# Optimization experiments

Hardware: AMD Instinct MI355X
Metric: run time of the kernel (lower is better)

## Reference

```python
import jax, jax.numpy as jnp
import numpy as np

D_K = 64
EPS = 1e-6


def setup_inputs() -> dict:
    key = jax.random.key(0)
    ks = jax.random.split(key, 6)
    B, S, D2, DV = 4, 2048, 1024, 64
    q = jax.random.normal(ks[0], (B, S, D2), dtype=jnp.float32)
    k = jax.random.normal(ks[1], (B, S, D2), dtype=jnp.float32)
    v = jax.random.normal(ks[2], (B, S, D2), dtype=jnp.float32)
    mask = jax.random.randint(ks[3], (B, S, S), 0, 2) == 1
    V = jax.random.normal(ks[4], (1, DV), dtype=jnp.float32)
    fc_w = jax.random.normal(ks[5], (D2, DV), dtype=jnp.float32) * (1.0 / np.sqrt(DV))
    fc_b = jnp.zeros((D2,), dtype=jnp.float32)
    ln_g = jnp.ones((D2,), dtype=jnp.float32)
    ln_b = jnp.zeros((D2,), dtype=jnp.float32)
    return {"q": q, "k": k, "v": v, "mask": mask, "V": V,
            "fc_w": fc_w, "fc_b": fc_b, "ln_g": ln_g, "ln_b": ln_b}


def _layer_norm(x, g, b):
    mu = jnp.mean(x, axis=-1, keepdims=True)
    var = jnp.var(x, axis=-1, keepdims=True)
    return (x - mu) * jax.lax.rsqrt(var + EPS) * g + b


def reference(q, k, v, mask, V, fc_w, fc_b, ln_g, ln_b):
    residual = q
    qn = _layer_norm(q, ln_g, ln_b)
    # scaled dot-product scores (no softmax in this variant)
    attn = jnp.einsum('bsd,btd->bst', qn / jnp.sqrt(jnp.float32(D_K)), k)
    attn = jnp.where(mask, 0.0, attn)  # masked_fill with 0
    # v_ = V broadcast over (batch, seq, key); attn @ v_ == row-sum outer V
    output = jnp.sum(attn, axis=-1, keepdims=True) * V  # [B,S,d_v]
    output = output @ fc_w.T + fc_b                     # [B,S,2*d_model]
    output = output + residual
    return (output, attn)
```

## Files before the change

### kernel.cpp

```cpp
#include <hip/hip_runtime.h>
#include <hip/hip_bf16.h>
#include <cstdint>

#define S_LEN 2048
#define D2_   1024
#define DV_   64
#define NB_   4

typedef __bf16 bf16x8 __attribute__((ext_vector_type(8)));
typedef float  f32x4  __attribute__((ext_vector_type(4)));
typedef int    i32x4  __attribute__((ext_vector_type(4)));

__device__ __forceinline__ unsigned short f2bf(float f) {
  union { float f; unsigned int u; } v; v.f = f;
  unsigned int r = v.u + 0x7fffu + ((v.u >> 16) & 1u);
  return (unsigned short)(r >> 16);
}

__device__ __forceinline__ void async16(const unsigned short* g, unsigned short* l) {
  __builtin_amdgcn_global_load_lds(
      (__attribute__((address_space(1))) void*)g,
      (__attribute__((address_space(3))) void*)l,
      16, 0, 0);
}

__global__ void __launch_bounds__(256) prep_kernel(
    const float* __restrict__ q, const float* __restrict__ k,
    const float* __restrict__ gam, const float* __restrict__ bet,
    const float* __restrict__ V, const float* __restrict__ fw,
    unsigned short* __restrict__ qn, unsigned short* __restrict__ kb,
    float* __restrict__ w2, float* __restrict__ rowsum) {
  const int row = blockIdx.x;
  const int t = threadIdx.x;

  if (row < 32) rowsum[row * 256 + t] = 0.0f;

  const float4 x = ((const float4*)(q + (size_t)row * D2_))[t];
  float s  = x.x + x.y + x.z + x.w;
  float ss = x.x * x.x + x.y * x.y + x.z * x.z + x.w * x.w;
  #pragma unroll
  for (int o = 32; o > 0; o >>= 1) { s += __shfl_down(s, o); ss += __shfl_down(ss, o); }
  __shared__ float red[8];
  if ((t & 63) == 0) { red[t >> 6] = s; red[(t >> 6) + 4] = ss; }
  __syncthreads();
  const float tot  = red[0] + red[1] + red[2] + red[3];
  const float tots = red[4] + red[5] + red[6] + red[7];
  const float mu  = tot * (1.0f / D2_);
  const float var = tots * (1.0f / D2_) - mu * mu;
  const float rs  = rsqrtf(var + 1e-6f) * 0.125f;
  const float4 gv = ((const float4*)gam)[t];
  const float4 bv = ((const float4*)bet)[t];
  ushort4 o4;
  o4.x = f2bf((x.x - mu) * rs * gv.x + 0.125f * bv.x);
  o4.y = f2bf((x.y - mu) * rs * gv.y + 0.125f * bv.y);
  o4.z = f2bf((x.z - mu) * rs * gv.z + 0.125f * bv.z);
  o4.w = f2bf((x.w - mu) * rs * gv.w + 0.125f * bv.w);
  ((ushort4*)(qn + (size_t)row * D2_))[t] = o4;

  const float4 kx = ((const float4*)(k + (size_t)row * D2_))[t];
  ushort4 k4;
  k4.x = f2bf(kx.x); k4.y = f2bf(kx.y); k4.z = f2bf(kx.z); k4.w = f2bf(kx.w);
  ((ushort4*)(kb + (size_t)row * D2_))[t] = k4;

  if (row < 4) {
    const int d = row * 256 + t;
    const float4* r  = (const float4*)(fw + (size_t)d * DV_);
    const float4* vv = (const float4*)V;
    float acc = 0.f;
    #pragma unroll
    for (int j = 0; j < 16; ++j) {
      const float4 a = r[j], b = vv[j];
      acc += a.x * b.x + a.y * b.y + a.z * b.z + a.w * b.w;
    }
    w2[d] = acc;
  }
}

__global__ void __launch_bounds__(256, 4) attn_gemm_kernel(
    const unsigned short* __restrict__ qn,
    const unsigned short* __restrict__ kb,
    const int* __restrict__ mask,
    float* __restrict__ attn,
    float* __restrict__ rowsum) {
  __shared__ __align__(16) unsigned short Asm_[8192];
  __shared__ __align__(16) unsigned short Bsm_[8192];

  const int t = threadIdx.x;

  const int orig = blockIdx.x + 16 * (blockIdx.y + 16 * blockIdx.z);
  const int swz  = (orig & 7) * 128 + (orig >> 3);
  const int bn = (swz & 15) * 128;
  const int bm = ((swz >> 4) & 15) * 128;
  const int bt = swz >> 8;

  const int srow_ = t >> 3;
  const int pg_   = (t & 7) ^ (srow_ & 7);
  const unsigned short* gA = qn + ((size_t)bt * S_LEN + bm + srow_) * D2_ + pg_ * 8;
  const unsigned short* gB = kb + ((size_t)bt * S_LEN + bn + srow_) * D2_ + pg_ * 8;
  unsigned short* lA = Asm_ + t * 8;
  unsigned short* lB = Bsm_ + t * 8;

  const int lane = t & 63;
  const int w  = t >> 6;
  const int wm = (w >> 1) * 64;
  const int wn = (w & 1) * 64;
  const int lr = lane & 15;
  const int lg = lane >> 4;

  #define STAGE(koff) do {                                          \
      _Pragma("unroll")                                             \
      for (int qq = 0; qq < 4; ++qq) {                              \
        async16(gA + (koff) + (size_t)qq * 32 * D2_, lA + qq * 2048); \
        async16(gB + (koff) + (size_t)qq * 32 * D2_, lB + qq * 2048); \
      }                                                             \
    } while (0)

  f32x4 acc[4][4] = {};

  STAGE(0);
  __syncthreads();

  #pragma unroll 1
  for (int kt = 0; kt < 16; ++kt) {
    #pragma unroll
    for (int ks = 0; ks < 2; ++ks) {
      const int sl = ((ks << 2) + lg) ^ (lr & 7);
      bf16x8 af[4], bfv[4];
      #pragma unroll
      for (int f = 0; f < 4; ++f)
        af[f]  = *(const bf16x8*)(Asm_ + (wm + f * 16 + lr) * 64 + sl * 8);
      #pragma unroll
      for (int f = 0; f < 4; ++f)
        bfv[f] = *(const bf16x8*)(Bsm_ + (wn + f * 16 + lr) * 64 + sl * 8);
      #pragma unroll
      for (int fm = 0; fm < 4; ++fm)
        #pragma unroll
        for (int fn = 0; fn < 4; ++fn)
          acc[fm][fn] = __builtin_amdgcn_mfma_f32_16x16x32_bf16(
              bfv[fn], af[fm], acc[fm][fn], 0, 0, 0);
    }
    __syncthreads();
    if (kt < 15) {
      STAGE((kt + 1) * 64);
      __syncthreads();
    }
  }

  const int m_base = bm + wm + lr;
  const size_t rb0 = ((size_t)bt * S_LEN) * S_LEN;
  #pragma unroll
  for (int fm = 0; fm < 4; ++fm) {
    const int m = m_base + fm * 16;
    const size_t rowbase = rb0 + (size_t)m * S_LEN;
    float s = 0.f;
    #pragma unroll
    for (int fn = 0; fn < 4; ++fn) {
      const int n0 = bn + wn + fn * 16 + lg * 4;
      const i32x4 mk = __builtin_nontemporal_load((const i32x4*)(mask + rowbase + n0));
      f32x4 v;
      v[0] = mk[0] ? 0.0f : acc[fm][fn][0];
      v[1] = mk[1] ? 0.0f : acc[fm][fn][1];
      v[2] = mk[2] ? 0.0f : acc[fm][fn][2];
      v[3] = mk[3] ? 0.0f : acc[fm][fn][3];
      *(f32x4*)(attn + rowbase + n0) = v;
      s += v[0] + v[1] + v[2] + v[3];
    }
    s += __shfl_xor(s, 16);
    s += __shfl_xor(s, 32);
    if (lane < 16) atomicAdd(rowsum + (size_t)bt * S_LEN + m, s);
  }
  #undef STAGE
}

__global__ void __launch_bounds__(256) out_kernel(
    const float* __restrict__ rowsum, const float* __restrict__ q,
    const float* __restrict__ w2, const float* __restrict__ fcb,
    float* __restrict__ out) {
  const int row = blockIdx.x;
  const int t = threadIdx.x;
  const float rs = rowsum[row];
  const float4 wv = ((const float4*)w2)[t];
  const float4 bv = ((const float4*)fcb)[t];
  const float4 qv = ((const float4*)(q + (size_t)row * D2_))[t];
  float4 o4;
  o4.x = rs * wv.x + bv.x + qv.x;
  o4.y = rs * wv.y + bv.y + qv.y;
  o4.z = rs * wv.z + bv.z + qv.z;
  o4.w = rs * wv.w + bv.w + qv.w;
  ((float4*)(out + (size_t)row * D2_))[t] = o4;
}

extern "C" void kernel_launch(void* const* d_in, const int* in_sizes, int n_in,
                              void* d_out, int out_size, void* d_ws, size_t ws_size,
                              hipStream_t stream) {
  (void)in_sizes; (void)n_in; (void)out_size; (void)ws_size;
  const float* q    = (const float*)d_in[0];
  const float* k    = (const float*)d_in[1];
  const int*   mask = (const int*)d_in[3];
  const float* V    = (const float*)d_in[4];
  const float* fw   = (const float*)d_in[5];
  const float* fcb  = (const float*)d_in[6];
  const float* lg   = (const float*)d_in[7];
  const float* lb   = (const float*)d_in[8];

  float* out  = (float*)d_out;
  float* attn = out + (size_t)NB_ * S_LEN * D2_;

  unsigned short* qn = (unsigned short*)out;
  unsigned short* kb = qn + (size_t)NB_ * S_LEN * D2_;
  float* w2     = (float*)d_ws;
  float* rowsum = w2 + D2_;

  prep_kernel<<<NB_ * S_LEN, 256, 0, stream>>>(q, k, lg, lb, V, fw, qn, kb, w2, rowsum);
  attn_gemm_kernel<<<dim3(S_LEN / 128, S_LEN / 128, NB_), 256, 0, stream>>>(qn, kb, mask, attn, rowsum);
  out_kernel<<<NB_ * S_LEN, 256, 0, stream>>>(rowsum, q, w2, fcb, out);
}
```

Baseline: 265.5 us.

## Double-buffer LDS tiles in attention GEMM to overlap loads with MFMA

Doubles the LDS buffers for the A and B tiles and prefetches the next k-tile into the alternate buffer while computing the current one. The loop waits with explicit vmcnt counts and raw barriers instead of full __syncthreads around each stage. This is meant to hide global-to-LDS load latency behind MFMA work. In exchange it doubles LDS use and lowers the occupancy hint from 4 to 2 blocks per CU, and it relies on vmcnt accounting for async LDS loads being correct.

Measured after the change: 269.8 us. About the same (+1.6%).

```diff
diff --git a/kernel.cpp b/kernel.cpp
--- a/kernel.cpp
+++ b/kernel.cpp
@@ -76,14 +76,14 @@
   }
 }
 
-__global__ void __launch_bounds__(256, 4) attn_gemm_kernel(
+__global__ void __launch_bounds__(256, 2) attn_gemm_kernel(
     const unsigned short* __restrict__ qn,
     const unsigned short* __restrict__ kb,
     const int* __restrict__ mask,
     float* __restrict__ attn,
     float* __restrict__ rowsum) {
-  __shared__ __align__(16) unsigned short Asm_[8192];
-  __shared__ __align__(16) unsigned short Bsm_[8192];
+  __shared__ __align__(16) unsigned short Asm_[2 * 8192];
+  __shared__ __align__(16) unsigned short Bsm_[2 * 8192];
 
   const int t = threadIdx.x;
 
@@ -107,31 +107,27 @@
   const int lr = lane & 15;
   const int lg = lane >> 4;
 
-  #define STAGE(koff) do {                                          \
+  #define STAGE(buf, koff) do {                                     \
       _Pragma("unroll")                                             \
       for (int qq = 0; qq < 4; ++qq) {                              \
-        async16(gA + (koff) + (size_t)qq * 32 * D2_, lA + qq * 2048); \
-        async16(gB + (koff) + (size_t)qq * 32 * D2_, lB + qq * 2048); \
+        async16(gA + (koff) + (size_t)qq * 32 * D2_, lA + (buf) + qq * 2048); \
+        async16(gB + (koff) + (size_t)qq * 32 * D2_, lB + (buf) + qq * 2048); \
       }                                                             \
     } while (0)
 
   f32x4 acc[4][4] = {};
 
-  STAGE(0);
-  __syncthreads();
-
-  #pragma unroll 1
-  for (int kt = 0; kt < 16; ++kt) {
+  auto compute = [&](int pl) {
     #pragma unroll
     for (int ks = 0; ks < 2; ++ks) {
       const int sl = ((ks << 2) + lg) ^ (lr & 7);
       bf16x8 af[4], bfv[4];
       #pragma unroll
       for (int f = 0; f < 4; ++f)
-        af[f]  = *(const bf16x8*)(Asm_ + (wm + f * 16 + lr) * 64 + sl * 8);
+        af[f]  = *(const bf16x8*)(Asm_ + pl + (wm + f * 16 + lr) * 64 + sl * 8);
       #pragma unroll
       for (int f = 0; f < 4; ++f)
-        bfv[f] = *(const bf16x8*)(Bsm_ + (wn + f * 16 + lr) * 64 + sl * 8);
+        bfv[f] = *(const bf16x8*)(Bsm_ + pl + (wn + f * 16 + lr) * 64 + sl * 8);
       #pragma unroll
       for (int fm = 0; fm < 4; ++fm)
         #pragma unroll
@@ -139,12 +135,23 @@
           acc[fm][fn] = __builtin_amdgcn_mfma_f32_16x16x32_bf16(
               bfv[fn], af[fm], acc[fm][fn], 0, 0, 0);
     }
-    __syncthreads();
-    if (kt < 15) {
-      STAGE((kt + 1) * 64);
-      __syncthreads();
-    }
+  };
+
+  STAGE(0, 0);
+  STAGE(8192, 64);
+
+  #pragma unroll 1
+  for (int kt = 0; kt < 15; ++kt) {
+    const int cur = (kt & 1) * 8192;
+    asm volatile("s_waitcnt vmcnt(8)" ::: "memory");
+    __builtin_amdgcn_s_barrier();
+    compute(cur);
+    __builtin_amdgcn_s_barrier();
+    if (kt < 14) STAGE(cur, (kt + 2) * 64);
   }
+  asm volatile("s_waitcnt vmcnt(0)" ::: "memory");
+  __builtin_amdgcn_s_barrier();
+  compute(8192);
 
   const int m_base = bm + wm + lr;
   const size_t rb0 = ((size_t)bt * S_LEN) * S_LEN;
```
